# Kernel optimization log

Hardware: AMD Instinct MI355X
Metric: run time of the kernel (lower is better)

The kernel has to match this reference:

```python
import jax, jax.numpy as jnp
import numpy as np

SIGMA = 1.0
CONST = 0.5 * np.log(2.0 * np.pi * SIGMA ** 2)  # scalar constant from __init__


def setup_inputs() -> dict:
    key = jax.random.key(0)
    k1, k2 = jax.random.split(key)
    predicted_points = jax.random.normal(k1, (4, 4096, 3), dtype=jnp.float32)
    gt_means = jax.random.normal(k2, (4, 4096, 3), dtype=jnp.float32)
    return {"predicted_points": predicted_points, "gt_means": gt_means}


def reference(predicted_points, gt_means):
    # pairwise squared distances: (B, N, M)
    diff = predicted_points[:, :, None, :] - gt_means[:, None, :, :]  # (B,N,M,D)
    sq_distances = jnp.sum(diff * diff, axis=-1)
    log_probs = -CONST - sq_distances / (2.0 * SIGMA ** 2)
    # stable logsumexp over mixture components M
    log_likelihood = jax.nn.logsumexp(log_probs, axis=2)  # (B, N)
    loss = -jnp.mean(log_likelihood)
    return loss
```

## Files before the change

### kernel.cpp

```cpp
#include <hip/hip_runtime.h>
#include <hip/hip_fp16.h>
#include <math.h>

#define BATCH 4
#define NPTS 4096
#define NMIX 4096
#define THREADS 1024
#define PPB 32
#define NBLOCKS ((BATCH * NPTS) / PPB)
#define NTILES (NMIX / 32)
#define NWAVES 16
#define TPW (NTILES / NWAVES)

#define LN2 0.6931471805599453f
#define CONST_TERM 0.9189385332046727f
#define INV_COUNT (1.0f / (float)(BATCH * NPTS))
#define SQK      3478.8221f
#define B4VAL    32768.0f
#define A4BASE   32497.587f
#define A4SLOPE  (-184.66497f)

typedef _Float16 f16x4 __attribute__((ext_vector_type(4)));
typedef float f32x16 __attribute__((ext_vector_type(16)));

__device__ __forceinline__ float fast_log2(float x) {
#if __has_builtin(__builtin_amdgcn_logf)
  return __builtin_amdgcn_logf(x);
#else
  return log2f(x);
#endif
}

__device__ __forceinline__ uint32_t pack_h2(float a, float b) {
  __half2 h = __float22half2_rn(make_float2(a, b));
  return __builtin_bit_cast(uint32_t, h);
}

__global__ __launch_bounds__(THREADS) void gm_main(
    const float* __restrict__ pred, const float* __restrict__ gt,
    float* __restrict__ bsum) {
  __shared__ __align__(8) uint2 gsh[NMIX];
  __shared__ float comb[NWAVES][PPB];

  const int t = threadIdx.x;
  const int b = blockIdx.x >> 7;
  const int n0 = (blockIdx.x & 127) * PPB;
  const int lane = t & 63;
  const int w = t >> 6;

#pragma unroll
  for (int i = 0; i < NMIX / (2 * THREADS); ++i) {
    int s = t + i * THREADS;
    const float2* g = (const float2*)(gt + ((size_t)(b * NMIX + 2 * s)) * 3);
    float2 g01 = g[0], g23 = g[1], g45 = g[2];
    float n20 = fmaf(g01.x, g01.x, fmaf(g01.y, g01.y, g23.x * g23.x));
    float n21 = fmaf(g23.y, g23.y, fmaf(g45.x, g45.x, g45.y * g45.y));
    float a40 = fmaf(n20, A4SLOPE, A4BASE);
    float a41 = fmaf(n21, A4SLOPE, A4BASE);
    gsh[2 * s] = make_uint2(pack_h2(SQK * g01.x, SQK * g01.y),
                            pack_h2(SQK * g23.x, a40));
    gsh[2 * s + 1] = make_uint2(pack_h2(SQK * g23.y, SQK * g45.x),
                                pack_h2(SQK * g45.y, a41));
  }

  f16x4 afrag;
  {
    uint2 au = make_uint2(0u, 0u);
    if (lane < 32) {
      const float* p = pred + (size_t)(b * NPTS + n0 + lane) * 3;
      au = make_uint2(pack_h2(SQK * p[0], SQK * p[1]),
                      pack_h2(SQK * p[2], B4VAL));
    }
    afrag = __builtin_bit_cast(f16x4, au);
  }

  __syncthreads();

  f32x16 acc = 0.0f;
  {
    const uint2* bbase = gsh + w * (TPW * 32) + (lane & 31);
    const bool lo = lane < 32;
    const f32x16 czero = 0.0f;
#pragma unroll 4
    for (int j = 0; j < TPW; ++j) {
      uint2 raw = bbase[j * 32];
      raw.x = lo ? raw.x : 0u;
      raw.y = lo ? raw.y : 0u;
      f16x4 bfrag = __builtin_bit_cast(f16x4, raw);
      f32x16 d = __builtin_amdgcn_mfma_f32_32x32x8f16(afrag, bfrag, czero, 0, 0, 0);
#pragma unroll
      for (int r = 0; r < 16; ++r)
        acc[r] += __builtin_bit_cast(float, (int)d[r]);
    }
  }

#pragma unroll
  for (int mask = 1; mask <= 16; mask <<= 1) {
#pragma unroll
    for (int r = 0; r < 16; ++r) acc[r] += __shfl_xor(acc[r], mask, 64);
  }

  if ((lane & 31) == 0) {
#pragma unroll
    for (int r = 0; r < 16; ++r)
      comb[w][(r & 3) + 8 * (r >> 2) + 4 * (lane >> 5)] = acc[r];
  }
  __syncthreads();

  if (t < PPB) {
    float s = 0.f;
#pragma unroll
    for (int ww = 0; ww < NWAVES; ++ww) s += comb[ww][t];
    const float* p = pred + (size_t)(b * NPTS + n0 + t) * 3;
    float hp2 = 0.5f * (p[0] * p[0] + p[1] * p[1] + p[2] * p[2]);
    float ll = (LN2 * fast_log2(s) - hp2) * INV_COUNT;
#pragma unroll
    for (int off = 16; off > 0; off >>= 1) ll += __shfl_down(ll, off, 32);
    if (t == 0) bsum[blockIdx.x] = ll;
  }
}

__global__ __launch_bounds__(256) void gm_reduce(
    const float* __restrict__ bsum, float* __restrict__ out) {
  const int t = threadIdx.x;
  float v = bsum[t] + bsum[t + 256];
  for (int off = 32; off > 0; off >>= 1) v += __shfl_down(v, off, 64);
  __shared__ float w[4];
  if ((t & 63) == 0) w[t >> 6] = v;
  __syncthreads();
  if (t == 0) out[0] = CONST_TERM - ((w[0] + w[1]) + (w[2] + w[3]));
}

extern "C" void kernel_launch(void* const* d_in, const int* in_sizes, int n_in,
                              void* d_out, int out_size, void* d_ws, size_t ws_size,
                              hipStream_t stream) {
  const float* pred = (const float*)d_in[0];
  const float* gt   = (const float*)d_in[1];
  float* out = (float*)d_out;
  float* bsum = (float*)d_ws;

  gm_main<<<NBLOCKS, THREADS, 0, stream>>>(pred, gt, bsum);
  gm_reduce<<<1, 256, 0, stream>>>(bsum, out);
}
```

Measured before the change: 18.08 us.

## Split mixture dimension across two blocks and combine partial sums in final kernel

Splits the mixture-component axis into two halves so each block handles 32 points against 2048 components using 512 threads, which doubles the grid to 1024 blocks. Per-point partial exp-sums are written to workspace, and the final single-block kernel adds the halves, takes the log and reduces. The aim is higher occupancy and more parallelism, with smaller shared staging per block. In exchange it adds a global round-trip of 32K floats and a heavier final reduction.

```diff
diff --git a/kernel.cpp b/kernel.cpp
--- a/kernel.cpp
+++ b/kernel.cpp
@@ -5,12 +5,13 @@
 #define BATCH 4
 #define NPTS 4096
 #define NMIX 4096
-#define THREADS 1024
+#define THREADS 512
 #define PPB 32
-#define NBLOCKS ((BATCH * NPTS) / PPB)
-#define NTILES (NMIX / 32)
-#define NWAVES 16
-#define TPW (NTILES / NWAVES)
+#define NTILE 512
+#define NBLOCKS 1024
+#define MHALF 2048
+#define NWAVES 8
+#define TPW (MHALF / 32 / NWAVES)
 
 #define LN2 0.6931471805599453f
 #define CONST_TERM 0.9189385332046727f
@@ -38,20 +39,24 @@
 
 __global__ __launch_bounds__(THREADS) void gm_main(
     const float* __restrict__ pred, const float* __restrict__ gt,
-    float* __restrict__ bsum) {
-  __shared__ __align__(8) uint2 gsh[NMIX];
+    float* __restrict__ pp, float* __restrict__ aux) {
+  __shared__ __align__(8) uint2 gsh[MHALF];
   __shared__ float comb[NWAVES][PPB];
 
   const int t = threadIdx.x;
-  const int b = blockIdx.x >> 7;
-  const int n0 = (blockIdx.x & 127) * PPB;
+  const int z = blockIdx.x >> 9;
+  const int tile = blockIdx.x & 511;
+  const int b = tile >> 7;
+  const int n0 = (tile & 127) * PPB;
+  const int m0 = z * MHALF;
   const int lane = t & 63;
   const int w = t >> 6;
 
 #pragma unroll
-  for (int i = 0; i < NMIX / (2 * THREADS); ++i) {
+  for (int i = 0; i < MHALF / (2 * THREADS); ++i) {
     int s = t + i * THREADS;
-    const float2* g = (const float2*)(gt + ((size_t)(b * NMIX + 2 * s)) * 3);
+    const float2* g =
+        (const float2*)(gt + ((size_t)(b * NMIX + m0 + 2 * s)) * 3);
     float2 g01 = g[0], g23 = g[1], g45 = g[2];
     float n20 = fmaf(g01.x, g01.x, fmaf(g01.y, g01.y, g23.x * g23.x));
     float n21 = fmaf(g23.y, g23.y, fmaf(g45.x, g45.x, g45.y * g45.y));
@@ -108,27 +113,47 @@
   __syncthreads();
 
   if (t < PPB) {
-    float s = 0.f;
+    float s = ((comb[0][t] + comb[1][t]) + (comb[2][t] + comb[3][t])) +
+              ((comb[4][t] + comb[5][t]) + (comb[6][t] + comb[7][t]));
+    pp[(size_t)z * (BATCH * NPTS) + tile * PPB + t] = s;
+
+    if (z == 0) {
+      const float* p = pred + (size_t)(b * NPTS + n0 + t) * 3;
+      float hp2 = 0.5f * (p[0] * p[0] + p[1] * p[1] + p[2] * p[2]);
 #pragma unroll
-    for (int ww = 0; ww < NWAVES; ++ww) s += comb[ww][t];
-    const float* p = pred + (size_t)(b * NPTS + n0 + t) * 3;
-    float hp2 = 0.5f * (p[0] * p[0] + p[1] * p[1] + p[2] * p[2]);
-    float ll = (LN2 * fast_log2(s) - hp2) * INV_COUNT;
-#pragma unroll
-    for (int off = 16; off > 0; off >>= 1) ll += __shfl_down(ll, off, 32);
-    if (t == 0) bsum[blockIdx.x] = ll;
+      for (int off = 16; off > 0; off >>= 1)
+        hp2 += __shfl_down(hp2, off, 32);
+      if (t == 0) aux[tile] = hp2;
+    }
   }
 }
 
-__global__ __launch_bounds__(256) void gm_reduce(
-    const float* __restrict__ bsum, float* __restrict__ out) {
+__global__ __launch_bounds__(1024) void gm_final(
+    const float* __restrict__ pp, const float* __restrict__ aux,
+    float* __restrict__ out) {
   const int t = threadIdx.x;
-  float v = bsum[t] + bsum[t + 256];
-  for (int off = 32; off > 0; off >>= 1) v += __shfl_down(v, off, 64);
-  __shared__ float w[4];
-  if ((t & 63) == 0) w[t >> 6] = v;
+  const float* pp0 = pp;
+  const float* pp1 = pp + BATCH * NPTS;
+
+  float part = 0.f;
+#pragma unroll
+  for (int i = 0; i < (BATCH * NPTS) / 1024; ++i) {
+    int idx = t + i * 1024;
+    part += fast_log2(pp0[idx] + pp1[idx]);
+  }
+  part *= LN2;
+  if (t < NTILE) part -= aux[t];
+
+  for (int off = 32; off > 0; off >>= 1) part += __shfl_down(part, off, 64);
+  __shared__ float wred[16];
+  if ((t & 63) == 0) wred[t >> 6] = part;
   __syncthreads();
-  if (t == 0) out[0] = CONST_TERM - ((w[0] + w[1]) + (w[2] + w[3]));
+  if (t < 16) {
+    float v = wred[t];
+#pragma unroll
+    for (int off = 8; off > 0; off >>= 1) v += __shfl_down(v, off, 16);
+    if (t == 0) out[0] = CONST_TERM - v * INV_COUNT;
+  }
 }
 
 extern "C" void kernel_launch(void* const* d_in, const int* in_sizes, int n_in,
@@ -137,8 +162,9 @@
   const float* pred = (const float*)d_in[0];
   const float* gt   = (const float*)d_in[1];
   float* out = (float*)d_out;
-  float* bsum = (float*)d_ws;
+  float* pp  = (float*)d_ws;
+  float* aux = pp + 2 * (BATCH * NPTS);
 
-  gm_main<<<NBLOCKS, THREADS, 0, stream>>>(pred, gt, bsum);
-  gm_reduce<<<1, 256, 0, stream>>>(bsum, out);
+  gm_main<<<NBLOCKS, THREADS, 0, stream>>>(pred, gt, pp, aux);
+  gm_final<<<1, 1024, 0, stream>>>(pp, aux, out);
 }
```

Result: slower. 18.89 us (+4.5%).
